# Kernel optimization log

Hardware: AMD Instinct MI355X
Metric: run time of the kernel (lower is better)

## Reference

```python
import jax, jax.numpy as jnp
import numpy as np
from math import sqrt

EMBED_DIM = 1024
NUM_HEADS = 16
HEAD_DIM = EMBED_DIM // NUM_HEADS  # 64
SCALE = sqrt(HEAD_DIM)


def _rotate_half(x):
    # matches torch: stack((-x[...,1::2], x[...,0::2]), -1).flatten(-2)
    x1 = x[..., 0::2]
    x2 = x[..., 1::2]
    return jnp.stack((-x2, x1), axis=-1).reshape(x.shape)


def _apply_rope(x, seq_len):
    # x: [B, H, S, D]
    inv_freq = 1.0 / (10000.0 ** (jnp.arange(0, HEAD_DIM, 2, dtype=jnp.float32) / HEAD_DIM))
    pos = jnp.arange(seq_len, dtype=jnp.float32)
    freqs = jnp.outer(pos, inv_freq)            # [S, D/2]
    emb = jnp.concatenate([freqs, freqs], -1)   # [S, D]
    cos = jnp.cos(emb)[None, None].astype(x.dtype)
    sin = jnp.sin(emb)[None, None].astype(x.dtype)
    return x * cos + _rotate_half(x) * sin


def setup_inputs() -> dict:
    key = jax.random.key(0)
    ks = jax.random.split(key, 9)
    B, S, E = 2, 2048, EMBED_DIM
    s = 1.0 / np.sqrt(E)
    return {
        "x": jax.random.normal(ks[0], (B, S, E), jnp.float32),
        "Wq": jax.random.uniform(ks[1], (E, E), jnp.float32, -s, s),
        "bq": jnp.zeros((E,), jnp.float32),
        "Wk": jax.random.uniform(ks[2], (E, E), jnp.float32, -s, s),
        "bk": jnp.zeros((E,), jnp.float32),
        "Wv": jax.random.uniform(ks[3], (E, E), jnp.float32, -s, s),
        "bv": jnp.zeros((E,), jnp.float32),
        "Wo": jax.random.uniform(ks[4], (E, E), jnp.float32, -s, s),
        "bo": jnp.zeros((E,), jnp.float32),
    }


def reference(x, Wq, bq, Wk, bk, Wv, bv, Wo, bo):
    B, S, E = x.shape
    H, D = NUM_HEADS, HEAD_DIM
    # projections (torch Linear: x @ W.T + b), split heads -> [B, H, S, D]
    q = (x @ Wq.T + bq).reshape(B, S, H, D).transpose(0, 2, 1, 3)
    k = (x @ Wk.T + bk).reshape(B, S, H, D).transpose(0, 2, 1, 3)
    v = (x @ Wv.T + bv).reshape(B, S, H, D).transpose(0, 2, 1, 3)
    q = _apply_rope(q, S)
    k = _apply_rope(k, S)
    attn = jnp.einsum("bhqd,bhkd->bhqk", q, k) / SCALE
    attn = jax.nn.softmax(attn, axis=-1)
    out = jnp.einsum("bhqk,bhkd->bhqd", attn, v)
    out = out.transpose(0, 2, 1, 3).reshape(B, S, E)
    return out @ Wo.T + bo
```

## Files before the change

kernel.cpp:

```cpp
#include <hip/hip_runtime.h>
#include <hip/hip_bf16.h>
#include <math.h>

typedef __bf16 bf16;
typedef __bf16 bf16x4 __attribute__((ext_vector_type(4)));
typedef __bf16 bf16x8 __attribute__((ext_vector_type(8)));
typedef float f32x4 __attribute__((ext_vector_type(4)));

#define SEQ  2048
#define EMB  1024
#define NH   16
#define HD   64
#define MTOT 4096

__device__ __forceinline__ void gl_lds16(const void* g, void* l) {
  __builtin_amdgcn_global_load_lds(
      (const __attribute__((address_space(1))) void*)g,
      (__attribute__((address_space(3))) void*)l, 16, 0, 0);
}

__device__ __forceinline__ f32x4 mfma16(bf16x8 a, bf16x8 b, f32x4 c) {
  return __builtin_amdgcn_mfma_f32_16x16x32_bf16(a, b, c, 0, 0, 0);
}

#define ROPE_C 0.41524101186092026f
#define QSCL  0.1803368801111244f

__global__ __launch_bounds__(256) void cvt_all_kernel(
    const float* __restrict__ x,
    const float* __restrict__ w0, const float* __restrict__ w1,
    const float* __restrict__ w2, const float* __restrict__ w3,
    bf16* __restrict__ dst) {
  const int y = blockIdx.y;
  const size_t WN = (size_t)EMB * EMB;
  const float* src = (y < 4) ? (x + (size_t)y * WN)
                   : (y == 4) ? w0 : (y == 5) ? w1 : (y == 6) ? w2 : w3;
  size_t i = ((size_t)blockIdx.x * 256 + threadIdx.x) * 8;
  float4 a = *(const float4*)(src + i);
  float4 b = *(const float4*)(src + i + 4);
  bf16x8 o;
  o[0] = (bf16)a.x; o[1] = (bf16)a.y; o[2] = (bf16)a.z; o[3] = (bf16)a.w;
  o[4] = (bf16)b.x; o[5] = (bf16)b.y; o[6] = (bf16)b.z; o[7] = (bf16)b.w;
  *(bf16x8*)(dst + (size_t)y * WN + i) = o;
}

__global__ __launch_bounds__(256) void gemm_kernel(
    const bf16* __restrict__ X,
    const bf16* __restrict__ W0, const bf16* __restrict__ W1, const bf16* __restrict__ W2,
    const float* __restrict__ B0, const float* __restrict__ B1, const float* __restrict__ B2,
    bf16* __restrict__ Oq, bf16* __restrict__ Ok, bf16* __restrict__ Ovt)
{
  const int K = EMB;
  const int tid  = threadIdx.x;
  const int lane = tid & 63;
  const int w    = tid >> 6;
  const int wm   = w >> 1, wn = w & 1;
  const int tile_n = blockIdx.x * 128;
  const int tile_m = blockIdx.y * 128;
  const int z = blockIdx.z;
  const bf16*  Wsel = (z == 0) ? W0 : (z == 1 ? W1 : W2);
  const float* Bsel = (z == 0) ? B0 : (z == 1 ? B1 : B2);

  __shared__ __align__(16) unsigned char smem[128 * 132 * 2];
  bf16* As = (bf16*)smem;
  bf16* Bs = (bf16*)(smem + 8192);

  f32x4 acc[4][4];
#pragma unroll
  for (int i = 0; i < 4; i++)
#pragma unroll
    for (int j = 0; j < 4; j++) acc[i][j] = f32x4{0.f, 0.f, 0.f, 0.f};

  const int quad = lane >> 4;
  const int l15  = lane & 15;
  const int srow = lane >> 2;
  const int scl  = lane & 3;

  for (int k0 = 0; k0 < K; k0 += 32) {
#pragma unroll
    for (int i = 0; i < 2; i++) {
      int r = i * 64 + w * 16 + srow;
      int c = scl ^ ((r >> 1) & 3);
      gl_lds16(X    + (size_t)(tile_m + r) * K + k0 + c * 8, As + (i * 64 + w * 16) * 32);
      gl_lds16(Wsel + (size_t)(tile_n + r) * K + k0 + c * 8, Bs + (i * 64 + w * 16) * 32);
    }
    __syncthreads();

    bf16x8 af[4], bfr[4];
#pragma unroll
    for (int mt = 0; mt < 4; mt++) {
      int ml = wm * 64 + mt * 16 + l15;
      af[mt] = *(const bf16x8*)(As + ml * 32 + (quad ^ ((ml >> 1) & 3)) * 8);
    }
#pragma unroll
    for (int nt = 0; nt < 4; nt++) {
      int nl = wn * 64 + nt * 16 + l15;
      bfr[nt] = *(const bf16x8*)(Bs + nl * 32 + (quad ^ ((nl >> 1) & 3)) * 8);
    }
#pragma unroll
    for (int mt = 0; mt < 4; mt++)
#pragma unroll
      for (int nt = 0; nt < 4; nt++)
        acc[mt][nt] = mfma16(af[mt], bfr[nt], acc[mt][nt]);
    __syncthreads();
  }

  bf16* CS = (bf16*)smem;
  const int b = tile_m >> 11;
  const int s0 = tile_m & (SEQ - 1);

  if (z < 2) {
#pragma unroll
    for (int nt = 0; nt < 4; nt++) {
      const int nl = wn * 64 + nt * 16 + l15;
      const int n = tile_n + nl;
      const float bias = Bsel[n];
      const int j = n & 31;
      const float invf = exp2f(-(float)j * ROPE_C);
#pragma unroll
      for (int mt = 0; mt < 4; mt++) {
#pragma unroll
        for (int r = 0; r < 4; r++) {
          const int ml = wm * 64 + mt * 16 + quad * 4 + r;
          float a = acc[mt][nt][r] + bias;
          float p = __shfl_xor(a, 1, 64);
          float th = (float)((s0 + ml) & (SEQ - 1)) * invf;
          float sn, cs;
          __sincosf(th, &sn, &cs);
          float res = (n & 1) ? fmaf(p, sn, a * cs) : fmaf(-p, sn, a * cs);
          if (z == 0) res *= QSCL;
          CS[ml * 132 + nl] = (bf16)res;
        }
      }
    }
    __syncthreads();
    bf16* Odst = (z == 0) ? Oq : Ok;
#pragma unroll
    for (int g = 0; g < 8; g++) {
      int unit = g * 256 + tid;
      int chunk = unit & 7;
      int row = unit >> 3;
      int hl = row >> 7, sl = row & 127;
      bf16x8 v = *(const bf16x8*)(CS + sl * 132 + hl * 64 + chunk * 8);
      int hg = (tile_n >> 6) + hl;
      size_t o = ((size_t)(b * NH + hg) * SEQ + s0 + sl) * HD + chunk * 8;
      *(bf16x8*)(Odst + o) = v;
    }
  } else {
#pragma unroll
    for (int nt = 0; nt < 4; nt++) {
      const int nl = wn * 64 + nt * 16 + l15;
      const float bias = Bsel[tile_n + nl];
#pragma unroll
      for (int mt = 0; mt < 4; mt++) {
        const int mb = wm * 64 + mt * 16 + quad * 4;
#pragma unroll
        for (int r = 0; r < 4; r++)
          CS[nl * 132 + mb + r] = (bf16)(acc[mt][nt][r] + bias);
      }
    }
    __syncthreads();
#pragma unroll
    for (int g = 0; g < 8; g++) {
      int unit = g * 256 + tid;
      int chunk = unit & 15;
      int row = unit >> 4;
      bf16x8 v = *(const bf16x8*)(CS + row * 132 + chunk * 8);
      int nglob = tile_n + row;
      int d = nglob & 63, hg = nglob >> 6;
      size_t o = ((size_t)(b * NH + hg) * HD + d) * SEQ + s0 + chunk * 8;
      *(bf16x8*)(Ovt + o) = v;
    }
  }
}

__global__ __launch_bounds__(256) void gemm_o_kernel(
    const bf16* __restrict__ X,
    const bf16* __restrict__ W,
    const float* __restrict__ Bb,
    float* __restrict__ Out)
{
  const int tid = threadIdx.x, lane = tid & 63, w = tid >> 6;
  const int tile_n = blockIdx.x * 128;
  const int tile_m = blockIdx.y * 64;
  __shared__ __align__(16) bf16 As[64 * 32];
  __shared__ __align__(16) bf16 Bs[128 * 32];

  f32x4 acc[4][2];
#pragma unroll
  for (int i = 0; i < 4; i++)
#pragma unroll
    for (int j = 0; j < 2; j++) acc[i][j] = f32x4{0.f, 0.f, 0.f, 0.f};

  const int quad = lane >> 4, l15 = lane & 15;
  const int srow = lane >> 2, scl = lane & 3;

  for (int k0 = 0; k0 < EMB; k0 += 32) {
    {
      int r = w * 16 + srow;
      int c = scl ^ ((r >> 1) & 3);
      gl_lds16(X + (size_t)(tile_m + r) * EMB + k0 + c * 8, As + (w * 16) * 32);
    }
#pragma unroll
    for (int i = 0; i < 2; i++) {
      int r = i * 64 + w * 16 + srow;
      int c = scl ^ ((r >> 1) & 3);
      gl_lds16(W + (size_t)(tile_n + r) * EMB + k0 + c * 8, Bs + (i * 64 + w * 16) * 32);
    }
    __syncthreads();

    bf16x8 af[4], bfr[2];
#pragma unroll
    for (int mt = 0; mt < 4; mt++) {
      int ml = mt * 16 + l15;
      af[mt] = *(const bf16x8*)(As + ml * 32 + (quad ^ ((ml >> 1) & 3)) * 8);
    }
#pragma unroll
    for (int nt = 0; nt < 2; nt++) {
      int nl = w * 32 + nt * 16 + l15;
      bfr[nt] = *(const bf16x8*)(Bs + nl * 32 + (quad ^ ((nl >> 1) & 3)) * 8);
    }
#pragma unroll
    for (int mt = 0; mt < 4; mt++)
#pragma unroll
      for (int nt = 0; nt < 2; nt++)
        acc[mt][nt] = mfma16(af[mt], bfr[nt], acc[mt][nt]);
    __syncthreads();
  }

#pragma unroll
  for (int nt = 0; nt < 2; nt++) {
    const int n = tile_n + w * 32 + nt * 16 + l15;
    const float bias = Bb[n];
#pragma unroll
    for (int mt = 0; mt < 4; mt++) {
#pragma unroll
      for (int r = 0; r < 4; r++) {
        const int m = tile_m + mt * 16 + quad * 4 + r;
        Out[(size_t)m * EMB + n] = acc[mt][nt][r] + bias;
      }
    }
  }
}

__global__ __launch_bounds__(256) void flash_kernel(
    const bf16* __restrict__ Q,
    const bf16* __restrict__ Kk,
    const bf16* __restrict__ Vt,
    bf16* __restrict__ O)
{
  const int bh = blockIdx.y;
  const int qt = blockIdx.x;
  const int tid = threadIdx.x, lane = tid & 63, w = tid >> 6;
  const int quad = lane >> 4, l15 = lane & 15;

  __shared__ __align__(16) unsigned char smem[65536];

  const bf16* qbase = Q  + (size_t)bh * SEQ * HD;
  const bf16* kbase = Kk + (size_t)bh * SEQ * HD;
  const bf16* vbase = Vt + (size_t)bh * HD * SEQ;

  auto stage = [&](int kt, int buf) {
    bf16* Ks = (bf16*)(smem + buf * 32768);
    bf16* Vs = Ks + 8192;
#pragma unroll
    for (int i = 0; i < 4; i++) {
      int r = w * 32 + i * 8 + (lane >> 3);
      int c = (lane & 7) ^ (r & 7);
      gl_lds16(kbase + (size_t)(kt * 128 + r) * HD + c * 8, Ks + (w * 32 + i * 8) * 64);
      int dv = w * 16 + i * 4 + (lane >> 4);
      int cv = (lane & 15) ^ (dv & 15);
      gl_lds16(vbase + (size_t)dv * SEQ + kt * 128 + cv * 8, Vs + (w * 16 + i * 4) * 128);
    }
  };

  stage(0, 0);

  bf16x8 qf[2][2];
#pragma unroll
  for (int m = 0; m < 2; m++)
#pragma unroll
    for (int t = 0; t < 2; t++)
      qf[m][t] = *(const bf16x8*)(qbase + (size_t)(qt * 128 + w * 32 + m * 16 + l15) * HD
                                  + t * 32 + quad * 8);

  float lsum[2] = {0.f, 0.f};
  f32x4 oacc[2][4];
#pragma unroll
  for (int m = 0; m < 2; m++)
#pragma unroll
    for (int i = 0; i < 4; i++) oacc[m][i] = f32x4{0.f, 0.f, 0.f, 0.f};

  __syncthreads();

  for (int kt = 0; kt < SEQ / 128; kt++) {
    const int buf = kt & 1;
    if (kt + 1 < SEQ / 128) stage(kt + 1, buf ^ 1);
    const bf16* Ks = (const bf16*)(smem + buf * 32768);
    const bf16* Vs = Ks + 8192;

#pragma unroll
    for (int t2 = 0; t2 < 4; t2++) {
      bf16x8 pa[2];
#pragma unroll
      for (int hh = 0; hh < 2; hh++) {
        const int krow = (t2 * 2 + hh) * 16 + l15;
        const int swz = krow & 7;
        bf16x8 kf0 = *(const bf16x8*)(Ks + krow * 64 + ((quad ^ swz) & 7) * 8);
        bf16x8 kf1 = *(const bf16x8*)(Ks + krow * 64 + (((4 + quad) ^ swz) & 7) * 8);
#pragma unroll
        for (int mq = 0; mq < 2; mq++) {
          f32x4 s = f32x4{0.f, 0.f, 0.f, 0.f};
          s = mfma16(kf0, qf[mq][0], s);
          s = mfma16(kf1, qf[mq][1], s);
#pragma unroll
          for (int r = 0; r < 4; r++) {
            float p = __builtin_amdgcn_exp2f(s[r]);
            lsum[mq] += p;
            pa[mq][hh * 4 + r] = (bf16)p;
          }
        }
      }
#pragma unroll
      for (int dt = 0; dt < 4; dt++) {
        const int d = dt * 16 + l15;
        const bf16* vrow = Vs + d * 128 + (quad & 1) * 4;
        const int G = t2 * 4 + (quad >> 1);
        bf16x4 va = *(const bf16x4*)(vrow + ((G ^ l15) & 15) * 8);
        bf16x4 vb = *(const bf16x4*)(vrow + (((G + 2) ^ l15) & 15) * 8);
        bf16x8 vv = __builtin_shufflevector(va, vb, 0, 1, 2, 3, 4, 5, 6, 7);
#pragma unroll
        for (int mq = 0; mq < 2; mq++)
          oacc[mq][dt] = mfma16(vv, pa[mq], oacc[mq][dt]);
      }
    }
    __syncthreads();
  }

  float rls[2];
#pragma unroll
  for (int mq = 0; mq < 2; mq++) {
    float s = lsum[mq];
    s += __shfl_xor(s, 16, 64);
    s += __shfl_xor(s, 32, 64);
    rls[mq] = __builtin_amdgcn_rcpf(s);
  }

  const int b = bh >> 4, h = bh & 15;
#pragma unroll
  for (int mq = 0; mq < 2; mq++) {
    const int srow = qt * 128 + w * 32 + mq * 16 + l15;
    bf16* orow = O + ((size_t)(b * SEQ + srow)) * EMB + h * HD;
#pragma unroll
    for (int dt = 0; dt < 4; dt++) {
      bf16x4 ov;
#pragma unroll
      for (int r = 0; r < 4; r++) ov[r] = (bf16)(oacc[mq][dt][r] * rls[mq]);
      *(bf16x4*)(orow + dt * 16 + quad * 4) = ov;
    }
  }
}

extern "C" void kernel_launch(void* const* d_in, const int* in_sizes, int n_in,
                              void* d_out, int out_size, void* d_ws, size_t ws_size,
                              hipStream_t stream) {
  const float* x  = (const float*)d_in[0];
  const float* Wq = (const float*)d_in[1];
  const float* bq = (const float*)d_in[2];
  const float* Wk = (const float*)d_in[3];
  const float* bk = (const float*)d_in[4];
  const float* Wv = (const float*)d_in[5];
  const float* bv = (const float*)d_in[6];
  const float* Wo = (const float*)d_in[7];
  const float* bo = (const float*)d_in[8];

  const size_t XN = (size_t)MTOT * EMB;
  const size_t WN = (size_t)EMB * EMB;

  bf16* xb = (bf16*)d_ws;
  bf16* wq = xb + XN;
  bf16* wk = wq + WN;
  bf16* wv = wk + WN;
  bf16* wo = wv + WN;
  bf16* q  = wo + WN;
  bf16* k  = q + XN;
  bf16* vt = k + XN;
  bf16* at = vt + XN;
  float* out = (float*)d_out;

  dim3 blk(256);
  cvt_all_kernel<<<dim3(512, 8), blk, 0, stream>>>(x, Wq, Wk, Wv, Wo, xb);

  gemm_kernel<<<dim3(8, 32, 3), blk, 0, stream>>>(
      xb, wq, wk, wv, bq, bk, bv, q, k, vt);
  flash_kernel<<<dim3(16, 32), blk, 0, stream>>>(q, k, vt, at);
  gemm_o_kernel<<<dim3(8, 64), blk, 0, stream>>>(at, wo, bo, out);
}
```

Before: 205.0 us.

## Split flash attention keys across waves, register-prefetch K/V, reduce in LDS

Flash kernel now gives each block 64 query rows, with each of the 4 waves handling a disjoint key slice. K and V fragments are loaded directly from global memory into registers with double-buffered prefetch, replacing the LDS staging. Partial outputs and row sums are reduced across waves through shared memory at the end, and blocks are remapped with a swizzle for cache locality. The grid doubles and launch bounds target 2 blocks per CU. The V-projection epilogue also permutes the sequence order within 32-element groups to match the new V fragment layout. The cost is more global load traffic without LDS reuse, plus a final cross-wave reduction.

```diff
diff --git a/kernel.cpp b/kernel.cpp
--- a/kernel.cpp
+++ b/kernel.cpp
@@ -155,8 +155,11 @@
       for (int mt = 0; mt < 4; mt++) {
         const int mb = wm * 64 + mt * 16 + quad * 4;
 #pragma unroll
-        for (int r = 0; r < 4; r++)
-          CS[nl * 132 + mb + r] = (bf16)(acc[mt][nt][r] + bias);
+        for (int r = 0; r < 4; r++) {
+          const int ml = mb + r;
+          const int mp = (ml & ~31) | ((ml & 12) << 1) | ((ml & 16) >> 2) | (ml & 3);
+          CS[nl * 132 + mp] = (bf16)(acc[mt][nt][r] + bias);
+        }
       }
     }
     __syncthreads();
@@ -243,122 +246,153 @@
   }
 }
 
-__global__ __launch_bounds__(256) void flash_kernel(
+__global__ __launch_bounds__(256, 2) void flash_kernel(
     const bf16* __restrict__ Q,
     const bf16* __restrict__ Kk,
     const bf16* __restrict__ Vt,
     bf16* __restrict__ O)
 {
-  const int bh = blockIdx.y;
-  const int qt = blockIdx.x;
+  const int lin = blockIdx.x + blockIdx.y * 32;
+  const int sw  = (lin & 7) * 128 + (lin >> 3);
+  const int bh  = sw >> 5;
+  const int qt  = sw & 31;
   const int tid = threadIdx.x, lane = tid & 63, w = tid >> 6;
   const int quad = lane >> 4, l15 = lane & 15;
 
-  __shared__ __align__(16) unsigned char smem[65536];
+  __shared__ __align__(16) float osum[4][64][36];
+  __shared__ float lsd[4][4][16];
 
   const bf16* qbase = Q  + (size_t)bh * SEQ * HD;
   const bf16* kbase = Kk + (size_t)bh * SEQ * HD;
   const bf16* vbase = Vt + (size_t)bh * HD * SEQ;
 
-  auto stage = [&](int kt, int buf) {
-    bf16* Ks = (bf16*)(smem + buf * 32768);
-    bf16* Vs = Ks + 8192;
-#pragma unroll
-    for (int i = 0; i < 4; i++) {
-      int r = w * 32 + i * 8 + (lane >> 3);
-      int c = (lane & 7) ^ (r & 7);
-      gl_lds16(kbase + (size_t)(kt * 128 + r) * HD + c * 8, Ks + (w * 32 + i * 8) * 64);
-      int dv = w * 16 + i * 4 + (lane >> 4);
-      int cv = (lane & 15) ^ (dv & 15);
-      gl_lds16(vbase + (size_t)dv * SEQ + kt * 128 + cv * 8, Vs + (w * 16 + i * 4) * 128);
-    }
-  };
-
-  stage(0, 0);
-
-  bf16x8 qf[2][2];
-#pragma unroll
-  for (int m = 0; m < 2; m++)
+  const bf16* kp  = kbase + (size_t)(w * 32 + l15) * HD + quad * 8;
+  const bf16* vp0 = vbase + (size_t)(0 * 16 + l15) * SEQ + w * 32 + quad * 8;
+  const bf16* vp1 = vbase + (size_t)(1 * 16 + l15) * SEQ + w * 32 + quad * 8;
+  const bf16* vp2 = vbase + (size_t)(2 * 16 + l15) * SEQ + w * 32 + quad * 8;
+  const bf16* vp3 = vbase + (size_t)(3 * 16 + l15) * SEQ + w * 32 + quad * 8;
+
+  bf16x8 qf[4][2];
+#pragma unroll
+  for (int m = 0; m < 4; m++)
 #pragma unroll
     for (int t = 0; t < 2; t++)
-      qf[m][t] = *(const bf16x8*)(qbase + (size_t)(qt * 128 + w * 32 + m * 16 + l15) * HD
+      qf[m][t] = *(const bf16x8*)(qbase + (size_t)(qt * 64 + m * 16 + l15) * HD
                                   + t * 32 + quad * 8);
 
-  float lsum[2] = {0.f, 0.f};
-  f32x4 oacc[2][4];
-#pragma unroll
-  for (int m = 0; m < 2; m++)
+  float lsum[4] = {0.f, 0.f, 0.f, 0.f};
+  f32x4 oacc[4][4];
+#pragma unroll
+  for (int m = 0; m < 4; m++)
 #pragma unroll
     for (int i = 0; i < 4; i++) oacc[m][i] = f32x4{0.f, 0.f, 0.f, 0.f};
 
-  __syncthreads();
-
-  for (int kt = 0; kt < SEQ / 128; kt++) {
-    const int buf = kt & 1;
-    if (kt + 1 < SEQ / 128) stage(kt + 1, buf ^ 1);
-    const bf16* Ks = (const bf16*)(smem + buf * 32768);
-    const bf16* Vs = Ks + 8192;
-
-#pragma unroll
-    for (int t2 = 0; t2 < 4; t2++) {
-      bf16x8 pa[2];
-#pragma unroll
-      for (int hh = 0; hh < 2; hh++) {
-        const int krow = (t2 * 2 + hh) * 16 + l15;
-        const int swz = krow & 7;
-        bf16x8 kf0 = *(const bf16x8*)(Ks + krow * 64 + ((quad ^ swz) & 7) * 8);
-        bf16x8 kf1 = *(const bf16x8*)(Ks + krow * 64 + (((4 + quad) ^ swz) & 7) * 8);
-#pragma unroll
-        for (int mq = 0; mq < 2; mq++) {
-          f32x4 s = f32x4{0.f, 0.f, 0.f, 0.f};
-          s = mfma16(kf0, qf[mq][0], s);
-          s = mfma16(kf1, qf[mq][1], s);
-#pragma unroll
-          for (int r = 0; r < 4; r++) {
-            float p = __builtin_amdgcn_exp2f(s[r]);
-            lsum[mq] += p;
-            pa[mq][hh * 4 + r] = (bf16)p;
-          }
-        }
-      }
-#pragma unroll
-      for (int dt = 0; dt < 4; dt++) {
-        const int d = dt * 16 + l15;
-        const bf16* vrow = Vs + d * 128 + (quad & 1) * 4;
-        const int G = t2 * 4 + (quad >> 1);
-        bf16x4 va = *(const bf16x4*)(vrow + ((G ^ l15) & 15) * 8);
-        bf16x4 vb = *(const bf16x4*)(vrow + (((G + 2) ^ l15) & 15) * 8);
-        bf16x8 vv = __builtin_shufflevector(va, vb, 0, 1, 2, 3, 4, 5, 6, 7);
-#pragma unroll
-        for (int mq = 0; mq < 2; mq++)
-          oacc[mq][dt] = mfma16(vv, pa[mq], oacc[mq][dt]);
-      }
-    }
-    __syncthreads();
-  }
-
-  float rls[2];
-#pragma unroll
-  for (int mq = 0; mq < 2; mq++) {
-    float s = lsum[mq];
+  bf16x8 kA[2][2], kB[2][2], vA[4], vB[4];
+#define LOAD_KV(KD, VD)                                                       \
+  {                                                                           \
+    KD[0][0] = *(const bf16x8*)(kp);                                          \
+    KD[0][1] = *(const bf16x8*)(kp + 32);                                     \
+    KD[1][0] = *(const bf16x8*)(kp + 1024);                                   \
+    KD[1][1] = *(const bf16x8*)(kp + 1056);                                   \
+    VD[0] = *(const bf16x8*)(vp0);                                            \
+    VD[1] = *(const bf16x8*)(vp1);                                            \
+    VD[2] = *(const bf16x8*)(vp2);                                            \
+    VD[3] = *(const bf16x8*)(vp3);                                            \
+    kp += 8192; vp0 += 128; vp1 += 128; vp2 += 128; vp3 += 128;               \
+  }
+
+#define FLASH_STEP(KC, VC, KN, VN)                                            \
+  {                                                                           \
+    LOAD_KV(KN, VN);                                                          \
+    bf16x8 pa[4];                                                             \
+    _Pragma("unroll")                                                         \
+    for (int hh = 0; hh < 2; hh++) {                                          \
+      _Pragma("unroll")                                                       \
+      for (int m = 0; m < 4; m++) {                                           \
+        f32x4 s = f32x4{0.f, 0.f, 0.f, 0.f};                                  \
+        s = mfma16(KC[hh][0], qf[m][0], s);                                   \
+        s = mfma16(KC[hh][1], qf[m][1], s);                                   \
+        _Pragma("unroll")                                                     \
+        for (int r = 0; r < 4; r++) {                                         \
+          float p = __builtin_amdgcn_exp2f(s[r]);                             \
+          lsum[m] += p;                                                       \
+          pa[m][hh * 4 + r] = (bf16)p;                                        \
+        }                                                                     \
+      }                                                                       \
+    }                                                                         \
+    _Pragma("unroll")                                                         \
+    for (int dt = 0; dt < 4; dt++) {                                          \
+      _Pragma("unroll")                                                       \
+      for (int m = 0; m < 4; m++)                                             \
+        oacc[m][dt] = mfma16(VC[dt], pa[m], oacc[m][dt]);                     \
+    }                                                                         \
+  }
+
+  LOAD_KV(kA, vA);
+  for (int it = 0; it < SEQ / 256; it++) {
+    FLASH_STEP(kA, vA, kB, vB);
+    FLASH_STEP(kB, vB, kA, vA);
+  }
+
+#pragma unroll
+  for (int m = 0; m < 4; m++) {
+    float s = lsum[m];
     s += __shfl_xor(s, 16, 64);
     s += __shfl_xor(s, 32, 64);
-    rls[mq] = __builtin_amdgcn_rcpf(s);
-  }
+    if (quad == 0) lsd[w][m][l15] = s;
+  }
+#pragma unroll
+  for (int m = 0; m < 4; m++)
+#pragma unroll
+    for (int dl = 0; dl < 2; dl++)
+      *(f32x4*)&osum[w][m * 16 + l15][dl * 16 + quad * 4] = oacc[m][dl];
+  __syncthreads();
+
+  const float rls = __builtin_amdgcn_rcpf(
+      lsd[0][quad][l15] + lsd[1][quad][l15] + lsd[2][quad][l15] + lsd[3][quad][l15]);
 
   const int b = bh >> 4, h = bh & 15;
-#pragma unroll
-  for (int mq = 0; mq < 2; mq++) {
-    const int srow = qt * 128 + w * 32 + mq * 16 + l15;
-    bf16* orow = O + ((size_t)(b * SEQ + srow)) * EMB + h * HD;
-#pragma unroll
-    for (int dt = 0; dt < 4; dt++) {
-      bf16x4 ov;
-#pragma unroll
-      for (int r = 0; r < 4; r++) ov[r] = (bf16)(oacc[mq][dt][r] * rls[mq]);
-      *(bf16x4*)(orow + dt * 16 + quad * 4) = ov;
-    }
-  }
+  bf16* orow = O + (size_t)(b * SEQ + qt * 64 + lane) * EMB + h * HD;
+
+  {
+    f32x4 a0 = *(const f32x4*)&osum[0][lane][w * 8];
+    f32x4 a1 = *(const f32x4*)&osum[0][lane][w * 8 + 4];
+#pragma unroll
+    for (int wr = 1; wr < 4; wr++) {
+      a0 += *(const f32x4*)&osum[wr][lane][w * 8];
+      a1 += *(const f32x4*)&osum[wr][lane][w * 8 + 4];
+    }
+    a0 *= rls; a1 *= rls;
+    bf16x8 ov;
+#pragma unroll
+    for (int r = 0; r < 4; r++) { ov[r] = (bf16)a0[r]; ov[4 + r] = (bf16)a1[r]; }
+    *(bf16x8*)(orow + 0 * 32 + w * 8) = ov;
+  }
+  __syncthreads();
+
+#pragma unroll
+  for (int m = 0; m < 4; m++)
+#pragma unroll
+    for (int dl = 0; dl < 2; dl++)
+      *(f32x4*)&osum[w][m * 16 + l15][dl * 16 + quad * 4] = oacc[m][2 + dl];
+  __syncthreads();
+
+  {
+    f32x4 a0 = *(const f32x4*)&osum[0][lane][w * 8];
+    f32x4 a1 = *(const f32x4*)&osum[0][lane][w * 8 + 4];
+#pragma unroll
+    for (int wr = 1; wr < 4; wr++) {
+      a0 += *(const f32x4*)&osum[wr][lane][w * 8];
+      a1 += *(const f32x4*)&osum[wr][lane][w * 8 + 4];
+    }
+    a0 *= rls; a1 *= rls;
+    bf16x8 ov;
+#pragma unroll
+    for (int r = 0; r < 4; r++) { ov[r] = (bf16)a0[r]; ov[4 + r] = (bf16)a1[r]; }
+    *(bf16x8*)(orow + 1 * 32 + w * 8) = ov;
+  }
+#undef FLASH_STEP
+#undef LOAD_KV
 }
 
 extern "C" void kernel_launch(void* const* d_in, const int* in_sizes, int n_in,
@@ -393,6 +427,6 @@
 
   gemm_kernel<<<dim3(8, 32, 3), blk, 0, stream>>>(
       xb, wq, wk, wv, bq, bk, bv, q, k, vt);
-  flash_kernel<<<dim3(16, 32), blk, 0, stream>>>(q, k, vt, at);
+  flash_kernel<<<dim3(32, 32), blk, 0, stream>>>(q, k, vt, at);
   gemm_o_kernel<<<dim3(8, 64), blk, 0, stream>>>(at, wo, bo, out);
 }
```

Result: slower. 223.6 us (+9.1%).
